# Kernel tuning notes

Hardware: AMD Instinct MI355X
Metric: run time of the kernel (lower is better)

The kernel has to match this reference:

```python
import jax, jax.numpy as jnp
import numpy as np

N_NODES = 20000
N_EDGES = 320000
HIDDEN = 256
N_GRAPHS = 64
IN_DIM = 3
OUT_DIM = 2


def _glorot(key, shape):
    fan_in, fan_out = shape
    lim = jnp.sqrt(6.0 / (fan_in + fan_out))
    return jax.random.uniform(key, shape, jnp.float32, -lim, lim)


def setup_inputs() -> dict:
    key = jax.random.key(0)
    ks = jax.random.split(key, 16)
    inp = {
        "x": jax.random.normal(ks[0], (N_NODES, IN_DIM), jnp.float32),
        "edge_index": jax.random.randint(ks[1], (2, N_EDGES), 0, N_NODES, jnp.int64),
        "batch": jnp.sort(jax.random.randint(ks[2], (N_NODES,), 0, N_GRAPHS, jnp.int64)),
        "W1": _glorot(ks[3], (IN_DIM, HIDDEN)), "b1": jnp.zeros((HIDDEN,), jnp.float32),
        "W2": _glorot(ks[4], (HIDDEN, HIDDEN)), "b2": jnp.zeros((HIDDEN,), jnp.float32),
        "W3": _glorot(ks[5], (HIDDEN, HIDDEN)), "b3": jnp.zeros((HIDDEN,), jnp.float32),
        "W4": _glorot(ks[6], (HIDDEN, HIDDEN)), "b4": jnp.zeros((HIDDEN,), jnp.float32),
        "W5": _glorot(ks[7], (HIDDEN, HIDDEN)), "b5": jnp.zeros((HIDDEN,), jnp.float32),
        "Wlin": _glorot(ks[8], (HIDDEN, OUT_DIM)), "blin": jnp.zeros((OUT_DIM,), jnp.float32),
    }
    return inp


def _gcn_norm(edge_index, n_nodes):
    # PyG GCNConv default: add self-loops, symmetric degree normalization.
    loops = jnp.arange(n_nodes, dtype=edge_index.dtype)
    src = jnp.concatenate([edge_index[0], loops])
    dst = jnp.concatenate([edge_index[1], loops])
    deg = jax.ops.segment_sum(jnp.ones_like(dst, jnp.float32), dst, num_segments=n_nodes)
    dinv = jnp.where(deg > 0, jax.lax.rsqrt(deg), 0.0)
    norm = dinv[src] * dinv[dst]  # [E + N]
    return src, dst, norm


def _gcn_layer(x, W, b, src, dst, norm, n_nodes):
    h = x @ W                                   # [N, H]
    msg = h[src] * norm[:, None]                # [E+N, H] gather + scale
    agg = jax.ops.segment_sum(msg, dst, num_segments=n_nodes)  # scatter-add
    return agg + b


def reference(x, edge_index, batch, W1, b1, W2, b2, W3, b3, W4, b4, W5, b5, Wlin, blin):
    n = x.shape[0]
    src, dst, norm = _gcn_norm(edge_index, n)
    h = jax.nn.relu(_gcn_layer(x, W1, b1, src, dst, norm, n))
    h = jax.nn.relu(_gcn_layer(h, W2, b2, src, dst, norm, n))
    h = jax.nn.relu(_gcn_layer(h, W3, b3, src, dst, norm, n))
    h = jax.nn.relu(_gcn_layer(h, W4, b4, src, dst, norm, n))
    h = jax.nn.relu(_gcn_layer(h, W5, b5, src, dst, norm, n))
    pooled = jax.ops.segment_sum(h, batch, num_segments=N_GRAPHS)  # global_add_pool
    return pooled @ Wlin + blin
```

## Files before the change

### kernel.cpp

```cpp
#include <hip/hip_runtime.h>

#define N_NODES 20000
#define N_PAD 20032
#define N_EDGES 320000
#define HIDDEN 256
#define N_GRAPHS 64
#define OUT_DIM 2

#define PANEL_BYTES 131072
#define TABLE_BYTES 65536

typedef __attribute__((ext_vector_type(8))) short short8v;
typedef __attribute__((ext_vector_type(4))) float f32x4;
typedef __attribute__((ext_vector_type(4))) unsigned short us4;

__global__ void k_degree(const int* __restrict__ dst, int* __restrict__ degi) {
    int e = blockIdx.x * blockDim.x + threadIdx.x;
    if (e < N_EDGES) atomicAdd(&degi[dst[e]], 1);
}

__global__ void k_dinv(const int* __restrict__ degi, float* __restrict__ dinv) {
    int i = blockIdx.x * blockDim.x + threadIdx.x;
    if (i < N_NODES) dinv[i] = rsqrtf((float)degi[i] + 1.0f);
}

__global__ void k_scan(const int* __restrict__ degi, int* __restrict__ rowptr,
                       int* __restrict__ rowstart) {
    __shared__ int sums[1024];
    int t = threadIdx.x;
    int base = t * 20;
    int ld[20];
    int local = 0;
    if (t < 1000) {
#pragma unroll
        for (int i = 0; i < 20; ++i) { ld[i] = degi[base + i]; local += ld[i]; }
    }
    sums[t] = local;
    __syncthreads();
    for (int off = 1; off < 1024; off <<= 1) {
        int v = (t >= off) ? sums[t - off] : 0;
        __syncthreads();
        sums[t] += v;
        __syncthreads();
    }
    if (t < 1000) {
        int run = (t == 0) ? 0 : sums[t - 1];
#pragma unroll
        for (int i = 0; i < 20; ++i) {
            rowptr[base + i] = run;
            rowstart[base + i] = run;
            run += ld[i];
        }
    }
    if (t == 1023) rowptr[N_NODES] = sums[1023];
}

__global__ void k_fill(const int* __restrict__ src, const int* __restrict__ dst,
                       const float* __restrict__ dinv, int* __restrict__ rowstart,
                       int2* __restrict__ csr) {
    int e = blockIdx.x * blockDim.x + threadIdx.x;
    if (e >= N_EDGES) return;
    int s = src[e], d = dst[e];
    int pos = atomicAdd(&rowstart[d], 1);
    csr[pos] = make_int2(s, __float_as_int(dinv[s] * dinv[d]));
}

__global__ void k_wprep4(const float* __restrict__ W2, const float* __restrict__ W3,
                         const float* __restrict__ W4, const float* __restrict__ W5,
                         char* __restrict__ wt) {
    int lid = blockIdx.x >> 8;
    int idx = (blockIdx.x & 255) * 256 + threadIdx.x;
    const float* W = lid == 0 ? W2 : lid == 1 ? W3 : lid == 2 ? W4 : W5;
    int k = idx & 255, n = idx >> 8;
    float a = W[k * 256 + n];
    unsigned u = __float_as_uint(a);
    ushort hi = (ushort)(u >> 16);
    float hif = __uint_as_float(u & 0xffff0000u);
    ushort lo = (ushort)(__float_as_uint(a - hif) >> 16);
    int half = n >> 7, colL = n & 127, slab = k >> 3, e = k & 7;
    size_t base = ((size_t)lid * 2 + half) * PANEL_BYTES;
    size_t soff = (size_t)slab * 2048 + ((colL * 16 + slab * 32) & 2047) + e * 2;
    *(ushort*)(wt + base + soff) = hi;
    *(ushort*)(wt + base + TABLE_BYTES + soff) = lo;
}

__global__ void k_aggx(const float* __restrict__ x, const float* __restrict__ dinv,
                       const int* __restrict__ rowptr, const int2* __restrict__ csr,
                       float* __restrict__ z) {
    int i = blockIdx.x * blockDim.x + threadIdx.x;
    if (i >= N_NODES) return;
    float di = dinv[i];
    float w0 = di * di;
    float a0 = w0 * x[i * 3], a1 = w0 * x[i * 3 + 1], a2 = w0 * x[i * 3 + 2];
    float c0 = 0.f, c1 = 0.f, c2 = 0.f;
    int k = rowptr[i], end = rowptr[i + 1];
    for (; k + 1 < end; k += 2) {
        int2 e0 = csr[k], e1 = csr[k + 1];
        float we0 = __int_as_float(e0.y), we1 = __int_as_float(e1.y);
        const float* xs0 = x + (size_t)e0.x * 3;
        const float* xs1 = x + (size_t)e1.x * 3;
        a0 = fmaf(xs0[0], we0, a0);  c0 = fmaf(xs1[0], we1, c0);
        a1 = fmaf(xs0[1], we0, a1);  c1 = fmaf(xs1[1], we1, c1);
        a2 = fmaf(xs0[2], we0, a2);  c2 = fmaf(xs1[2], we1, c2);
    }
    if (k < end) {
        int2 e0 = csr[k];
        float we0 = __int_as_float(e0.y);
        const float* xs0 = x + (size_t)e0.x * 3;
        a0 = fmaf(xs0[0], we0, a0);
        a1 = fmaf(xs0[1], we0, a1);
        a2 = fmaf(xs0[2], we0, a2);
    }
    z[i * 3 + 0] = a0 + c0;
    z[i * 3 + 1] = a1 + c1;
    z[i * 3 + 2] = a2 + c2;
}

__global__ void k_h1(const float* __restrict__ z, const float* __restrict__ W1,
                     const float* __restrict__ b1,
                     ushort* __restrict__ out_hi, ushort* __restrict__ out_lo) {
    int i = blockIdx.x;
    int j = threadIdx.x;
    float z0 = z[i * 3], z1 = z[i * 3 + 1], z2 = z[i * 3 + 2];
    float v = fmaf(z0, W1[j], fmaf(z1, W1[256 + j], fmaf(z2, W1[512 + j], b1[j])));
    v = fmaxf(v, 0.0f);
    unsigned u = __float_as_uint(v);
    ushort hi = (ushort)(u >> 16);
    float hif = __uint_as_float(u & 0xffff0000u);
    ushort lo = (ushort)(__float_as_uint(v - hif) >> 16);
    out_hi[(size_t)i * HIDDEN + j] = hi;
    out_lo[(size_t)i * HIDDEN + j] = lo;
}

__global__ void k_csr_agg(const float* __restrict__ h, const float* __restrict__ dinv,
                          const int* __restrict__ rowptr, const int2* __restrict__ csr,
                          const float* __restrict__ b,
                          ushort* __restrict__ out_hi, ushort* __restrict__ out_lo) {
    int node = blockIdx.x * 4 + (threadIdx.x >> 6);
    if (node >= N_NODES) return;
    int lane = threadIdx.x & 63;
    int beg = rowptr[node], end = rowptr[node + 1];
    float di = dinv[node];
    float w0 = di * di;
    float4 bv = *reinterpret_cast<const float4*>(b + lane * 4);
    float4 hv = *reinterpret_cast<const float4*>(h + (size_t)node * HIDDEN + lane * 4);
    float4 A0, A1 = {0,0,0,0}, A2 = {0,0,0,0}, A3 = {0,0,0,0};
    A0.x = fmaf(hv.x, w0, bv.x);
    A0.y = fmaf(hv.y, w0, bv.y);
    A0.z = fmaf(hv.z, w0, bv.z);
    A0.w = fmaf(hv.w, w0, bv.w);
    int k = beg;
    for (; k + 3 < end; k += 4) {
        int2 e0 = csr[k], e1 = csr[k + 1], e2 = csr[k + 2], e3 = csr[k + 3];
        float we0 = __int_as_float(e0.y), we1 = __int_as_float(e1.y);
        float we2 = __int_as_float(e2.y), we3 = __int_as_float(e3.y);
        float4 v0 = *reinterpret_cast<const float4*>(h + (size_t)e0.x * HIDDEN + lane * 4);
        float4 v1 = *reinterpret_cast<const float4*>(h + (size_t)e1.x * HIDDEN + lane * 4);
        float4 v2 = *reinterpret_cast<const float4*>(h + (size_t)e2.x * HIDDEN + lane * 4);
        float4 v3 = *reinterpret_cast<const float4*>(h + (size_t)e3.x * HIDDEN + lane * 4);
        A0.x = fmaf(v0.x, we0, A0.x);  A1.x = fmaf(v1.x, we1, A1.x);
        A0.y = fmaf(v0.y, we0, A0.y);  A1.y = fmaf(v1.y, we1, A1.y);
        A0.z = fmaf(v0.z, we0, A0.z);  A1.z = fmaf(v1.z, we1, A1.z);
        A0.w = fmaf(v0.w, we0, A0.w);  A1.w = fmaf(v1.w, we1, A1.w);
        A2.x = fmaf(v2.x, we2, A2.x);  A3.x = fmaf(v3.x, we3, A3.x);
        A2.y = fmaf(v2.y, we2, A2.y);  A3.y = fmaf(v3.y, we3, A3.y);
        A2.z = fmaf(v2.z, we2, A2.z);  A3.z = fmaf(v3.z, we3, A3.z);
        A2.w = fmaf(v2.w, we2, A2.w);  A3.w = fmaf(v3.w, we3, A3.w);
    }
    for (; k < end; ++k) {
        int2 e0 = csr[k];
        float we0 = __int_as_float(e0.y);
        float4 v0 = *reinterpret_cast<const float4*>(h + (size_t)e0.x * HIDDEN + lane * 4);
        A0.x = fmaf(v0.x, we0, A0.x);
        A0.y = fmaf(v0.y, we0, A0.y);
        A0.z = fmaf(v0.z, we0, A0.z);
        A0.w = fmaf(v0.w, we0, A0.w);
    }
    float4 acc;
    acc.x = (A0.x + A1.x) + (A2.x + A3.x);
    acc.y = (A0.y + A1.y) + (A2.y + A3.y);
    acc.z = (A0.z + A1.z) + (A2.z + A3.z);
    acc.w = (A0.w + A1.w) + (A2.w + A3.w);
    float rv[4] = {fmaxf(acc.x, 0.f), fmaxf(acc.y, 0.f), fmaxf(acc.z, 0.f), fmaxf(acc.w, 0.f)};
    us4 hvv, lvv;
#pragma unroll
    for (int j = 0; j < 4; ++j) {
        unsigned u = __float_as_uint(rv[j]);
        hvv[j] = (ushort)(u >> 16);
        float hif = __uint_as_float(u & 0xffff0000u);
        lvv[j] = (ushort)(__float_as_uint(rv[j] - hif) >> 16);
    }
    *reinterpret_cast<us4*>(out_hi + (size_t)node * HIDDEN + lane * 4) = hvv;
    *reinterpret_cast<us4*>(out_lo + (size_t)node * HIDDEN + lane * 4) = lvv;
}

__global__ __launch_bounds__(512) void k_gemm_mfma(const ushort* __restrict__ a_hi,
                                                   const ushort* __restrict__ a_lo,
                                                   const char* __restrict__ wpanels,
                                                   float* __restrict__ out) {
    extern __shared__ char smem[];
    int bx = blockIdx.x;
    int half = bx & 1;
    int mtile = bx >> 1;
    const char* gsrc = wpanels + (size_t)half * PANEL_BYTES;
    int tid = threadIdx.x;
#pragma unroll
    for (int it = 0; it < 16; ++it) {
        int o = it * 8192 + tid * 16;
        *reinterpret_cast<float4*>(smem + o) = *reinterpret_cast<const float4*>(gsrc + o);
    }
    __syncthreads();

    int w = tid >> 6, l = tid & 63;
    int lr = l & 15, kg = l >> 4;
    int wm = w >> 2, wn = w & 3;
    int row0 = mtile * 64 + wm * 32;
    int colL0 = wn * 32;

    const ushort* aph = a_hi + (size_t)(row0 + lr) * HIDDEN + kg * 8;
    const ushort* apl = a_lo + (size_t)(row0 + lr) * HIDDEN + kg * 8;

    f32x4 acc[2][2] = {};
#pragma unroll
    for (int t = 0; t < 8; ++t) {
        int kb = t * 32;
        short8v ah0 = *reinterpret_cast<const short8v*>(aph + kb);
        short8v ah1 = *reinterpret_cast<const short8v*>(aph + 16 * HIDDEN + kb);
        short8v al0 = *reinterpret_cast<const short8v*>(apl + kb);
        short8v al1 = *reinterpret_cast<const short8v*>(apl + 16 * HIDDEN + kb);
        int slab = t * 4 + kg;
        int sbase = slab * 2048;
        int rot = slab * 32;
#pragma unroll
        for (int cf = 0; cf < 2; ++cf) {
            int colL = colL0 + cf * 16 + lr;
            int off = sbase + ((colL * 16 + rot) & 2047);
            short8v bh = *reinterpret_cast<const short8v*>(smem + off);
            short8v bl = *reinterpret_cast<const short8v*>(smem + TABLE_BYTES + off);
            acc[0][cf] = __builtin_amdgcn_mfma_f32_16x16x32_bf16(ah0, bh, acc[0][cf], 0, 0, 0);
            acc[1][cf] = __builtin_amdgcn_mfma_f32_16x16x32_bf16(ah1, bh, acc[1][cf], 0, 0, 0);
            acc[0][cf] = __builtin_amdgcn_mfma_f32_16x16x32_bf16(al0, bh, acc[0][cf], 0, 0, 0);
            acc[1][cf] = __builtin_amdgcn_mfma_f32_16x16x32_bf16(al1, bh, acc[1][cf], 0, 0, 0);
            acc[0][cf] = __builtin_amdgcn_mfma_f32_16x16x32_bf16(ah0, bl, acc[0][cf], 0, 0, 0);
            acc[1][cf] = __builtin_amdgcn_mfma_f32_16x16x32_bf16(ah1, bl, acc[1][cf], 0, 0, 0);
        }
    }
    int gcol = half * 128 + colL0 + lr;
#pragma unroll
    for (int rf = 0; rf < 2; ++rf) {
        float* orow = out + (size_t)(row0 + rf * 16 + kg * 4) * HIDDEN + gcol;
#pragma unroll
        for (int r = 0; r < 4; ++r)
#pragma unroll
            for (int cf = 0; cf < 2; ++cf)
                orow[(size_t)r * HIDDEN + cf * 16] = acc[rf][cf][r];
    }
}

__global__ void k_pool(const ushort* __restrict__ hi, const ushort* __restrict__ lo,
                       const int* __restrict__ batch, float* __restrict__ pooled) {
    int base = blockIdx.x * 32;
    int j = threadIdx.x;
    float acc = 0.0f;
    int cur = batch[base];
    for (int r = 0; r < 32; ++r) {
        int i = base + r;
        int bg = batch[i];
        if (bg != cur) {
            atomicAdd(&pooled[cur * HIDDEN + j], acc);
            acc = 0.0f;
            cur = bg;
        }
        size_t off = (size_t)i * HIDDEN + j;
        float v = __uint_as_float((unsigned)hi[off] << 16) +
                  __uint_as_float((unsigned)lo[off] << 16);
        acc += v;
    }
    atomicAdd(&pooled[cur * HIDDEN + j], acc);
}

__global__ void k_final(const float* __restrict__ pooled, const float* __restrict__ Wlin,
                        const float* __restrict__ blin, float* __restrict__ out) {
    int t = threadIdx.x;
    int g = t >> 1, o = t & 1;
    float s = blin[o];
    for (int k = 0; k < HIDDEN; ++k) s += pooled[g * HIDDEN + k] * Wlin[k * OUT_DIM + o];
    out[g * OUT_DIM + o] = s;
}

extern "C" void kernel_launch(void* const* d_in, const int* in_sizes, int n_in,
                              void* d_out, int out_size, void* d_ws, size_t ws_size,
                              hipStream_t stream) {
    const float* x     = (const float*)d_in[0];
    const int*   esrc  = (const int*)d_in[1];
    const int*   edst  = esrc + N_EDGES;
    const int*   batch = (const int*)d_in[2];
    const float* W1 = (const float*)d_in[3];
    const float* b1 = (const float*)d_in[4];
    const float* W2 = (const float*)d_in[5];
    const float* b2 = (const float*)d_in[6];
    const float* W3 = (const float*)d_in[7];
    const float* b3 = (const float*)d_in[8];
    const float* W4 = (const float*)d_in[9];
    const float* b4 = (const float*)d_in[10];
    const float* W5 = (const float*)d_in[11];
    const float* b5 = (const float*)d_in[12];
    const float* Wlin = (const float*)d_in[13];
    const float* blin = (const float*)d_in[14];
    float* out = (float*)d_out;

    char* ws = (char*)d_ws;
    size_t off = 0;
    auto alloc = [&](size_t bytes) { size_t o = off; off += (bytes + 255) & ~size_t(255); return (void*)(ws + o); };

    int*    degi     = (int*)alloc(N_NODES * 4);
    float*  dinv     = (float*)alloc(N_NODES * 4);
    int*    rowptr   = (int*)alloc((N_NODES + 1) * 4);
    int*    rowstart = (int*)alloc(N_NODES * 4);
    int2*   csr      = (int2*)alloc((size_t)N_EDGES * 8);
    float*  hA       = (float*)alloc((size_t)N_PAD * HIDDEN * 4);
    ushort* hb_hi    = (ushort*)alloc((size_t)N_PAD * HIDDEN * 2);
    ushort* hb_lo    = (ushort*)alloc((size_t)N_PAD * HIDDEN * 2);
    float*  pooled   = (float*)alloc(N_GRAPHS * HIDDEN * 4);
    char*   wt       = (char*)alloc((size_t)4 * 2 * PANEL_BYTES);
    float*  z        = (float*)alloc((size_t)N_NODES * 3 * 4);

    hipMemsetAsync(degi, 0, N_NODES * 4, stream);
    hipMemsetAsync(pooled, 0, N_GRAPHS * HIDDEN * 4, stream);

    k_degree<<<(N_EDGES + 255) / 256, 256, 0, stream>>>(edst, degi);
    k_dinv<<<(N_NODES + 255) / 256, 256, 0, stream>>>(degi, dinv);
    k_scan<<<1, 1024, 0, stream>>>(degi, rowptr, rowstart);
    k_fill<<<(N_EDGES + 255) / 256, 256, 0, stream>>>(esrc, edst, dinv, rowstart, csr);
    k_wprep4<<<1024, 256, 0, stream>>>(W2, W3, W4, W5, wt);

    const float* bs[5] = {b1, b2, b3, b4, b5};

    k_aggx<<<(N_NODES + 255) / 256, 256, 0, stream>>>(x, dinv, rowptr, csr, z);
    k_h1<<<N_NODES, HIDDEN, 0, stream>>>(z, W1, b1, hb_hi, hb_lo);

    for (int l = 1; l < 5; ++l) {
        k_gemm_mfma<<<(N_PAD / 64) * 2, 512, PANEL_BYTES, stream>>>(
            hb_hi, hb_lo, wt + (size_t)(l - 1) * 2 * PANEL_BYTES, hA);
        k_csr_agg<<<N_NODES / 4, 256, 0, stream>>>(hA, dinv, rowptr, csr, bs[l], hb_hi, hb_lo);
    }

    k_pool<<<N_NODES / 32, HIDDEN, 0, stream>>>(hb_hi, hb_lo, batch, pooled);
    k_final<<<1, 128, 0, stream>>>(pooled, Wlin, blin, out);
}
```

Before: 399.1 us.

## Make GEMM persistent to amortize weight-panel staging; fuse dinv into scan; parallelize aggx

The MFMA GEMM now runs as a persistent grid of 256 blocks. Each block loads its 128 KB weight panel into static shared memory once and then loops over 32-row tiles, so the panel is no longer reloaded by every 64-row tile. The dinv computation moves into the scan kernel, which removes one launch. The first-layer aggregation now uses one thread per node per feature instead of one thread per node, which raises parallelism. The risk is less latency hiding: each wave now computes only one 16-column fragment per tile, giving fewer MFMAs per A load, and tile counts may be imbalanced across blocks.

```diff
diff --git a/kernel.cpp b/kernel.cpp
--- a/kernel.cpp
+++ b/kernel.cpp
@@ -9,6 +9,7 @@
 
 #define PANEL_BYTES 131072
 #define TABLE_BYTES 65536
+#define NTILES 626
 
 typedef __attribute__((ext_vector_type(8))) short short8v;
 typedef __attribute__((ext_vector_type(4))) float f32x4;
@@ -19,13 +20,8 @@
     if (e < N_EDGES) atomicAdd(&degi[dst[e]], 1);
 }
 
-__global__ void k_dinv(const int* __restrict__ degi, float* __restrict__ dinv) {
-    int i = blockIdx.x * blockDim.x + threadIdx.x;
-    if (i < N_NODES) dinv[i] = rsqrtf((float)degi[i] + 1.0f);
-}
-
 __global__ void k_scan(const int* __restrict__ degi, int* __restrict__ rowptr,
-                       int* __restrict__ rowstart) {
+                       int* __restrict__ rowstart, float* __restrict__ dinv) {
     __shared__ int sums[1024];
     int t = threadIdx.x;
     int base = t * 20;
@@ -33,7 +29,11 @@
     int local = 0;
     if (t < 1000) {
 #pragma unroll
-        for (int i = 0; i < 20; ++i) { ld[i] = degi[base + i]; local += ld[i]; }
+        for (int i = 0; i < 20; ++i) {
+            ld[i] = degi[base + i];
+            local += ld[i];
+            dinv[base + i] = rsqrtf((float)ld[i] + 1.0f);
+        }
     }
     sums[t] = local;
     __syncthreads();
@@ -87,33 +87,22 @@
 __global__ void k_aggx(const float* __restrict__ x, const float* __restrict__ dinv,
                        const int* __restrict__ rowptr, const int2* __restrict__ csr,
                        float* __restrict__ z) {
-    int i = blockIdx.x * blockDim.x + threadIdx.x;
-    if (i >= N_NODES) return;
+    int t = blockIdx.x * blockDim.x + threadIdx.x;
+    int i = t >> 2, c = t & 3;
+    if (i >= N_NODES || c >= 3) return;
     float di = dinv[i];
-    float w0 = di * di;
-    float a0 = w0 * x[i * 3], a1 = w0 * x[i * 3 + 1], a2 = w0 * x[i * 3 + 2];
-    float c0 = 0.f, c1 = 0.f, c2 = 0.f;
+    float a = di * di * x[i * 3 + c], bacc = 0.f;
     int k = rowptr[i], end = rowptr[i + 1];
     for (; k + 1 < end; k += 2) {
         int2 e0 = csr[k], e1 = csr[k + 1];
-        float we0 = __int_as_float(e0.y), we1 = __int_as_float(e1.y);
-        const float* xs0 = x + (size_t)e0.x * 3;
-        const float* xs1 = x + (size_t)e1.x * 3;
-        a0 = fmaf(xs0[0], we0, a0);  c0 = fmaf(xs1[0], we1, c0);
-        a1 = fmaf(xs0[1], we0, a1);  c1 = fmaf(xs1[1], we1, c1);
-        a2 = fmaf(xs0[2], we0, a2);  c2 = fmaf(xs1[2], we1, c2);
+        a = fmaf(x[(size_t)e0.x * 3 + c], __int_as_float(e0.y), a);
+        bacc = fmaf(x[(size_t)e1.x * 3 + c], __int_as_float(e1.y), bacc);
     }
     if (k < end) {
         int2 e0 = csr[k];
-        float we0 = __int_as_float(e0.y);
-        const float* xs0 = x + (size_t)e0.x * 3;
-        a0 = fmaf(xs0[0], we0, a0);
-        a1 = fmaf(xs0[1], we0, a1);
-        a2 = fmaf(xs0[2], we0, a2);
-    }
-    z[i * 3 + 0] = a0 + c0;
-    z[i * 3 + 1] = a1 + c1;
-    z[i * 3 + 2] = a2 + c2;
+        a = fmaf(x[(size_t)e0.x * 3 + c], __int_as_float(e0.y), a);
+    }
+    z[i * 3 + c] = a + bacc;
 }
 
 __global__ void k_h1(const float* __restrict__ z, const float* __restrict__ W1,
@@ -198,10 +187,10 @@
                                                    const ushort* __restrict__ a_lo,
                                                    const char* __restrict__ wpanels,
                                                    float* __restrict__ out) {
-    extern __shared__ char smem[];
+    __shared__ char smem[PANEL_BYTES];
     int bx = blockIdx.x;
     int half = bx & 1;
-    int mtile = bx >> 1;
+    int bslot = bx >> 1;
     const char* gsrc = wpanels + (size_t)half * PANEL_BYTES;
     int tid = threadIdx.x;
 #pragma unroll
@@ -213,47 +202,38 @@
 
     int w = tid >> 6, l = tid & 63;
     int lr = l & 15, kg = l >> 4;
-    int wm = w >> 2, wn = w & 3;
-    int row0 = mtile * 64 + wm * 32;
-    int colL0 = wn * 32;
-
-    const ushort* aph = a_hi + (size_t)(row0 + lr) * HIDDEN + kg * 8;
-    const ushort* apl = a_lo + (size_t)(row0 + lr) * HIDDEN + kg * 8;
-
-    f32x4 acc[2][2] = {};
-#pragma unroll
-    for (int t = 0; t < 8; ++t) {
-        int kb = t * 32;
-        short8v ah0 = *reinterpret_cast<const short8v*>(aph + kb);
-        short8v ah1 = *reinterpret_cast<const short8v*>(aph + 16 * HIDDEN + kb);
-        short8v al0 = *reinterpret_cast<const short8v*>(apl + kb);
-        short8v al1 = *reinterpret_cast<const short8v*>(apl + 16 * HIDDEN + kb);
-        int slab = t * 4 + kg;
-        int sbase = slab * 2048;
-        int rot = slab * 32;
-#pragma unroll
-        for (int cf = 0; cf < 2; ++cf) {
-            int colL = colL0 + cf * 16 + lr;
-            int off = sbase + ((colL * 16 + rot) & 2047);
+    int colL = w * 16 + lr;
+    int gcol = half * 128 + colL;
+
+    for (int tile = bslot; tile < NTILES; tile += 128) {
+        int row0 = tile * 32;
+        const ushort* aph = a_hi + (size_t)(row0 + lr) * HIDDEN + kg * 8;
+        const ushort* apl = a_lo + (size_t)(row0 + lr) * HIDDEN + kg * 8;
+        f32x4 acc0 = {}, acc1 = {};
+#pragma unroll
+        for (int t = 0; t < 8; ++t) {
+            int kb = t * 32;
+            short8v ah0 = *reinterpret_cast<const short8v*>(aph + kb);
+            short8v ah1 = *reinterpret_cast<const short8v*>(aph + 16 * HIDDEN + kb);
+            short8v al0 = *reinterpret_cast<const short8v*>(apl + kb);
+            short8v al1 = *reinterpret_cast<const short8v*>(apl + 16 * HIDDEN + kb);
+            int slab = t * 4 + kg;
+            int off = slab * 2048 + ((colL * 16 + slab * 32) & 2047);
             short8v bh = *reinterpret_cast<const short8v*>(smem + off);
             short8v bl = *reinterpret_cast<const short8v*>(smem + TABLE_BYTES + off);
-            acc[0][cf] = __builtin_amdgcn_mfma_f32_16x16x32_bf16(ah0, bh, acc[0][cf], 0, 0, 0);
-            acc[1][cf] = __builtin_amdgcn_mfma_f32_16x16x32_bf16(ah1, bh, acc[1][cf], 0, 0, 0);
-            acc[0][cf] = __builtin_amdgcn_mfma_f32_16x16x32_bf16(al0, bh, acc[0][cf], 0, 0, 0);
-            acc[1][cf] = __builtin_amdgcn_mfma_f32_16x16x32_bf16(al1, bh, acc[1][cf], 0, 0, 0);
-            acc[0][cf] = __builtin_amdgcn_mfma_f32_16x16x32_bf16(ah0, bl, acc[0][cf], 0, 0, 0);
-            acc[1][cf] = __builtin_amdgcn_mfma_f32_16x16x32_bf16(ah1, bl, acc[1][cf], 0, 0, 0);
-        }
-    }
-    int gcol = half * 128 + colL0 + lr;
-#pragma unroll
-    for (int rf = 0; rf < 2; ++rf) {
-        float* orow = out + (size_t)(row0 + rf * 16 + kg * 4) * HIDDEN + gcol;
-#pragma unroll
-        for (int r = 0; r < 4; ++r)
-#pragma unroll
-            for (int cf = 0; cf < 2; ++cf)
-                orow[(size_t)r * HIDDEN + cf * 16] = acc[rf][cf][r];
+            acc0 = __builtin_amdgcn_mfma_f32_16x16x32_bf16(ah0, bh, acc0, 0, 0, 0);
+            acc1 = __builtin_amdgcn_mfma_f32_16x16x32_bf16(ah1, bh, acc1, 0, 0, 0);
+            acc0 = __builtin_amdgcn_mfma_f32_16x16x32_bf16(al0, bh, acc0, 0, 0, 0);
+            acc1 = __builtin_amdgcn_mfma_f32_16x16x32_bf16(al1, bh, acc1, 0, 0, 0);
+            acc0 = __builtin_amdgcn_mfma_f32_16x16x32_bf16(ah0, bl, acc0, 0, 0, 0);
+            acc1 = __builtin_amdgcn_mfma_f32_16x16x32_bf16(ah1, bl, acc1, 0, 0, 0);
+        }
+        float* o0 = out + (size_t)(row0 + kg * 4) * HIDDEN + gcol;
+#pragma unroll
+        for (int r = 0; r < 4; ++r) {
+            o0[(size_t)r * HIDDEN] = acc0[r];
+            o0[(size_t)(r + 16) * HIDDEN] = acc1[r];
+        }
     }
 }
 
@@ -329,18 +309,17 @@
     hipMemsetAsync(pooled, 0, N_GRAPHS * HIDDEN * 4, stream);
 
     k_degree<<<(N_EDGES + 255) / 256, 256, 0, stream>>>(edst, degi);
-    k_dinv<<<(N_NODES + 255) / 256, 256, 0, stream>>>(degi, dinv);
-    k_scan<<<1, 1024, 0, stream>>>(degi, rowptr, rowstart);
+    k_scan<<<1, 1024, 0, stream>>>(degi, rowptr, rowstart, dinv);
     k_fill<<<(N_EDGES + 255) / 256, 256, 0, stream>>>(esrc, edst, dinv, rowstart, csr);
     k_wprep4<<<1024, 256, 0, stream>>>(W2, W3, W4, W5, wt);
 
     const float* bs[5] = {b1, b2, b3, b4, b5};
 
-    k_aggx<<<(N_NODES + 255) / 256, 256, 0, stream>>>(x, dinv, rowptr, csr, z);
+    k_aggx<<<(N_NODES * 4 + 255) / 256, 256, 0, stream>>>(x, dinv, rowptr, csr, z);
     k_h1<<<N_NODES, HIDDEN, 0, stream>>>(z, W1, b1, hb_hi, hb_lo);
 
     for (int l = 1; l < 5; ++l) {
-        k_gemm_mfma<<<(N_PAD / 64) * 2, 512, PANEL_BYTES, stream>>>(
+        k_gemm_mfma<<<256, 512, 0, stream>>>(
             hb_hi, hb_lo, wt + (size_t)(l - 1) * 2 * PANEL_BYTES, hA);
         k_csr_agg<<<N_NODES / 4, 256, 0, stream>>>(hA, dinv, rowptr, csr, bs[l], hb_hi, hb_lo);
     }
```

After: 438.0 us. 9.7% more time.
